# Optimization experiments

Hardware: AMD Instinct MI355X
Metric: run time of the kernel (lower is better)

The kernel has to match this reference:

```python
import jax, jax.numpy as jnp
import numpy as np
import math

BZ, SEQ, NV, VA, HA = 16, 5, 1, 8, 8
C, DSTATE, DCONV, EXPAND, NLAYER = 384, 16, 4, 2, 4
DI = EXPAND * C
DTR = math.ceil(C / 16)  # 24
NTOK = (NV + 2) * SEQ * VA * HA  # 960 multi-modal tokens
T = NTOK + 2                     # + 2 gps tokens


def _ln(x, g, b, eps=1e-5):
    m = jnp.mean(x, -1, keepdims=True)
    v = jnp.mean((x - m) ** 2, -1, keepdims=True)
    return (x - m) * jax.lax.rsqrt(v + eps) * g + b


def _mamba(x, in_w, cw, cb, xw, dtw, dtb, a_log, d, ow):
    # x: (B,T,C); Mamba with bias=False in/out proj, conv_bias=True (mamba_ssm defaults)
    xz = jnp.einsum('btc,ec->bte', x, in_w)            # (B,T,2*DI)
    xh, z = jnp.split(xz, 2, axis=-1)
    xt = jnp.swapaxes(xh, 1, 2)                        # (B,DI,T)
    xt = jax.lax.conv_general_dilated(
        xt, cw[:, None, :], (1,), [(DCONV - 1, 0)],
        feature_group_count=DI, dimension_numbers=('NCH', 'OIH', 'NCH'))
    xh = jax.nn.silu(jnp.swapaxes(xt, 1, 2) + cb)      # causal depthwise conv + SiLU
    xdbl = jnp.einsum('btd,ed->bte', xh, xw)           # (B,T,DTR+2*DS)
    dt, Bm, Cm = jnp.split(xdbl, [DTR, DTR + DSTATE], axis=-1)
    dt = jax.nn.softplus(jnp.einsum('btr,dr->btd', dt, dtw) + dtb)  # (B,T,DI)
    A = -jnp.exp(a_log)                                # (DI,DSTATE)

    def step(h, inp):
        dt_t, x_t, b_t, c_t = inp                      # (B,DI),(B,DI),(B,DS),(B,DS)
        h = h * jnp.exp(dt_t[..., None] * A) + (dt_t * x_t)[..., None] * b_t[:, None, :]
        return h, jnp.einsum('bds,bs->bd', h, c_t)

    h0 = jnp.zeros((x.shape[0], DI, DSTATE), x.dtype)
    xs = tuple(jnp.swapaxes(a, 0, 1) for a in (dt, xh, Bm, Cm))
    _, ys = jax.lax.scan(step, h0, xs)
    y = jnp.swapaxes(ys, 0, 1) + d * xh
    y = y * jax.nn.silu(z)
    return jnp.einsum('btd,cd->btc', y, ow)


def _forward(image_tensor, lidar_tensor, radar_tensor, gps, pos_emb,
             ln1_g, ln1_b, fc1_w, fc1_b, fc2_w, fc2_b,
             in_proj_w, conv_w, conv_b, x_proj_w, dt_proj_w, dt_proj_b,
             A_log, D_param, out_proj_w, ln_f_g, ln_f_b):
    bz = lidar_tensor.shape[0] // SEQ
    h, w = lidar_tensor.shape[2], lidar_tensor.shape[3]
    img = image_tensor.reshape(bz, NV * SEQ, -1, h, w)
    lid = lidar_tensor.reshape(bz, SEQ, -1, h, w)
    rad = radar_tensor.reshape(bz, SEQ, -1, h, w)
    s1, s2 = C // 3, C // 3 * 2
    cs_img = jnp.concatenate([img[:, :, :s1], lid[:, :, s1:s2], rad[:, :, s2:]], axis=2)
    cs_lid = jnp.concatenate([lid[:, :, :s1], rad[:, :, s1:s2], img[:, :, s2:]], axis=2)
    cs_rad = jnp.concatenate([rad[:, :, :s1], img[:, :, s1:s2], lid[:, :, s2:]], axis=2)
    tok = jnp.concatenate([cs_img, cs_lid, cs_rad], axis=1)     # (bz, 3*SEQ, C, h, w)
    tok = jnp.transpose(tok, (0, 1, 3, 4, 2)).reshape(bz, -1, C)
    tok = jnp.concatenate([tok, gps], axis=1)                   # (bz, T, C)
    x = pos_emb + tok                                           # dropout is identity (eval)
    for l in range(NLAYER):
        x_ln = _ln(x, ln1_g[l], ln1_b[l])
        x_fc1 = jnp.einsum('btc,ec->bte', x_ln, fc1_w[l]) + fc1_b[l]
        x_fm = _mamba(x_fc1, in_proj_w[l, 0], conv_w[l, 0], conv_b[l, 0],
                      x_proj_w[l, 0], dt_proj_w[l, 0], dt_proj_b[l, 0],
                      A_log[l, 0], D_param[l, 0], out_proj_w[l, 0])
        x_flip = jnp.flip(x_fc1, axis=1)
        x_bm = _mamba(x_flip, in_proj_w[l, 1], conv_w[l, 1], conv_b[l, 1],
                      x_proj_w[l, 1], dt_proj_w[l, 1], dt_proj_b[l, 1],
                      A_log[l, 1], D_param[l, 1], out_proj_w[l, 1])
        x_fc2 = jnp.einsum('btc,ec->bte', x_flip, fc2_w[l]) + fc2_b[l]
        x_relu = jnp.where(x_fc2 >= 0, x_fc2, 0.2 * x_fc2)      # LeakyReLU(0.2)
        x = x_bm * x_relu + x_fm * x_bm                         # note: x_bm stays flipped, as in original
    x = _ln(x, ln_f_g, ln_f_b)
    pos_out = x[:, NTOK:]
    x = x[:, :NTOK].reshape(bz, (NV + 2) * SEQ, VA, HA, C)
    x = jnp.transpose(x, (0, 1, 4, 2, 3))
    img_out = x[:, :NV * SEQ].reshape(bz * NV * SEQ, -1, h, w)
    lid_out = x[:, NV * SEQ:(NV + 1) * SEQ].reshape(bz * SEQ, -1, h, w)
    rad_out = x[:, (NV + 1) * SEQ:].reshape(bz * SEQ, -1, h, w)
    return img_out, lid_out, rad_out, pos_out


def setup_inputs() -> dict:
    key = jax.random.key(0)
    it = iter(jax.random.split(key, 24))

    def n(shape, s=0.02):
        return jax.random.normal(next(it), shape, jnp.float32) * s

    return dict(
        image_tensor=n((BZ * NV * SEQ, C, VA, HA), 1.0),
        lidar_tensor=n((BZ * SEQ, C, VA, HA), 1.0),
        radar_tensor=n((BZ * SEQ, C, VA, HA), 1.0),
        gps=n((BZ, 2, C), 1.0),
        pos_emb=n((1, T, C), 0.02),
        ln1_g=jnp.ones((NLAYER, C)), ln1_b=jnp.zeros((NLAYER, C)),
        fc1_w=n((NLAYER, C, C)), fc1_b=jnp.zeros((NLAYER, C)),
        fc2_w=n((NLAYER, C, C)), fc2_b=jnp.zeros((NLAYER, C)),
        in_proj_w=n((NLAYER, 2, 2 * DI, C)),
        conv_w=n((NLAYER, 2, DI, DCONV), 0.1),
        conv_b=jnp.zeros((NLAYER, 2, DI)),
        x_proj_w=n((NLAYER, 2, DTR + 2 * DSTATE, DI)),
        dt_proj_w=n((NLAYER, 2, DI, DTR), 0.1),
        dt_proj_b=jnp.full((NLAYER, 2, DI), -4.6, jnp.float32),  # softplus ~ 0.01
        A_log=jnp.tile(jnp.log(jnp.arange(1., DSTATE + 1, dtype=jnp.float32)), (NLAYER, 2, DI, 1)),
        D_param=jnp.ones((NLAYER, 2, DI)),
        out_proj_w=n((NLAYER, 2, C, DI)),
        ln_f_g=jnp.ones((C,)), ln_f_b=jnp.zeros((C,)),
    )


def reference(image_tensor, lidar_tensor, radar_tensor, gps, pos_emb,
              ln1_g, ln1_b, fc1_w, fc1_b, fc2_w, fc2_b,
              in_proj_w, conv_w, conv_b, x_proj_w, dt_proj_w, dt_proj_b,
              A_log, D_param, out_proj_w, ln_f_g, ln_f_b):
    return _forward(image_tensor, lidar_tensor, radar_tensor, gps, pos_emb,
                    ln1_g, ln1_b, fc1_w, fc1_b, fc2_w, fc2_b,
                    in_proj_w, conv_w, conv_b, x_proj_w, dt_proj_w, dt_proj_b,
                    A_log, D_param, out_proj_w, ln_f_g, ln_f_b)
```

## Files before the change

### kernel.cpp

```cpp
#include <hip/hip_runtime.h>
#include <cstdint>
#include <cstddef>


constexpr int BZv = 16, SEQ = 5, NV = 1;
constexpr int C = 384, DSTATE = 16, DCONV = 4, NLAYER = 4;
constexpr int DI = 768;
constexpr int DTR = 24;
constexpr int NTOK = (NV + 2) * SEQ * 64;
constexpr int T = NTOK + 2;
constexpr int M = BZv * T;
constexpr int HB = 8;
constexpr int MH = HB * T;
constexpr int XZdim = 2 * DI;
constexpr int ND = DTR + 2 * DSTATE;
constexpr int NDP = 32;
constexpr int NCHUNK = 26, TC = 37;
constexpr int NQ = 241;
constexpr size_t SEC_SZ = (size_t)BZv * SEQ * C * 64;

typedef __attribute__((ext_vector_type(8))) short short8;
typedef __attribute__((ext_vector_type(4))) float floatx4;

#define GLOAD_LDS16(g, l)                                        \
  __builtin_amdgcn_global_load_lds(                              \
      (const __attribute__((address_space(1))) void*)(g),        \
      (__attribute__((address_space(3))) void*)(l), 16, 0, 0)

__device__ __forceinline__ void split_bf16(float v, short& hi, short& lo) {
  unsigned u = __float_as_uint(v);
  unsigned hib = u & 0xFFFF0000u;
  float r = v - __uint_as_float(hib);
  hi = (short)(hib >> 16);
  lo = (short)(__float_as_uint(r) >> 16);
}

__device__ __forceinline__ float join_bf16(short h, short l) {
  return __uint_as_float((unsigned)(unsigned short)h << 16) +
         __uint_as_float((unsigned)(unsigned short)l << 16);
}

__device__ __forceinline__ void pow16(float e1, float* e) {
  e[0] = e1;
  e[1] = e1 * e1;
  e[3] = e[1] * e[1];
  e[7] = e[3] * e[3];
  e[15] = e[7] * e[7];
  e[2] = e[1] * e[0];
  e[4] = e[3] * e[0];
  e[5] = e[3] * e[1];
  e[6] = e[5] * e[0];
  e[8] = e[7] * e[0];
  e[9] = e[7] * e[1];
  e[10] = e[9] * e[0];
  e[11] = e[7] * e[3];
  e[12] = e[11] * e[0];
  e[13] = e[11] * e[1];
  e[14] = e[13] * e[0];
}

__global__ __launch_bounds__(256) void assemble_k(
    const float* __restrict__ img, const float* __restrict__ lid,
    const float* __restrict__ rad, const float* __restrict__ gps,
    const float* __restrict__ pe, float* __restrict__ x) {
  int idx = blockIdx.x * 256 + threadIdx.x;
  int c = idx % C;
  int m = idx / C;
  int b = m / T, t = m - b * T;
  float v;
  if (t < NTOK) {
    int g_ = t >> 6, p = t & 63;
    int sec = g_ / 5, s = g_ % 5;
    int band = (c < 128) ? 0 : (c < 256 ? 1 : 2);
    int which = (band + sec) % 3;
    const float* src = (which == 0) ? img : (which == 1 ? lid : rad);
    v = src[(((size_t)(b * 5 + s) * C + c) << 6) + p];
  } else {
    v = gps[((size_t)b * 2 + (t - NTOK)) * C + c];
  }
  x[idx] = v + pe[(size_t)t * C + c];
}

__global__ __launch_bounds__(256) void ln_fused_k(
    const float* __restrict__ x, const float* __restrict__ g,
    const float* __restrict__ b, short* __restrict__ oh,
    short* __restrict__ ol) {
  int row = blockIdx.x * 4 + (threadIdx.x >> 6);
  int lane = threadIdx.x & 63;
  const float* xr = x + (size_t)row * C;
  float v[6];
  float s = 0.f;
#pragma unroll
  for (int j = 0; j < 6; j++) {
    v[j] = xr[lane + 64 * j];
    s += v[j];
  }
#pragma unroll
  for (int o = 32; o > 0; o >>= 1) s += __shfl_xor(s, o, 64);
  float mean = s * (1.f / 384.f);
  float q = 0.f;
#pragma unroll
  for (int j = 0; j < 6; j++) {
    float d = v[j] - mean;
    q += d * d;
  }
#pragma unroll
  for (int o = 32; o > 0; o >>= 1) q += __shfl_xor(q, o, 64);
  float rstd = rsqrtf(q * (1.f / 384.f) + 1e-5f);
#pragma unroll
  for (int j = 0; j < 6; j++) {
    int c = lane + 64 * j;
    float val = (v[j] - mean) * rstd * g[c] + b[c];
    short h, l;
    split_bf16(val, h, l);
    oh[(size_t)row * C + c] = h;
    ol[(size_t)row * C + c] = l;
  }
}

__global__ __launch_bounds__(256) void ln_stats2_k(const float* __restrict__ x,
                                                   float* __restrict__ stats) {
  int row = blockIdx.x * 4 + (threadIdx.x >> 6);
  int lane = threadIdx.x & 63;
  const float* xr = x + (size_t)row * C;
  float v[6];
  float s = 0.f;
#pragma unroll
  for (int j = 0; j < 6; j++) {
    v[j] = xr[lane + 64 * j];
    s += v[j];
  }
#pragma unroll
  for (int o = 32; o > 0; o >>= 1) s += __shfl_xor(s, o, 64);
  float mean = s * (1.f / 384.f);
  float q = 0.f;
#pragma unroll
  for (int j = 0; j < 6; j++) {
    float d = v[j] - mean;
    q += d * d;
  }
#pragma unroll
  for (int o = 32; o > 0; o >>= 1) q += __shfl_xor(q, o, 64);
  if (lane == 0) {
    stats[2 * row] = mean;
    stats[2 * row + 1] = rsqrtf(q * (1.f / 384.f) + 1e-5f);
  }
}

__global__ __launch_bounds__(256) void cast_k(const float* __restrict__ src,
                                              int n, short* __restrict__ oh,
                                              short* __restrict__ ol) {
  int idx = blockIdx.x * 256 + threadIdx.x;
  if (idx >= n) return;
  short h, l;
  split_bf16(src[idx], h, l);
  oh[idx] = h;
  ol[idx] = l;
}

__global__ __launch_bounds__(256) void cast_pad_k(const float* __restrict__ src,
                                                  int n, short* __restrict__ oh,
                                                  short* __restrict__ ol) {
  int idx = blockIdx.x * 256 + threadIdx.x;
  if (idx >= n) return;
  int col = idx & 31, row = idx >> 5;
  float v = (col < DTR) ? src[row * DTR + col] : 0.f;
  short h, l;
  split_bf16(v, h, l);
  oh[idx] = h;
  ol[idx] = l;
}

template <int ACT, bool BIAS, bool FLIPA, bool OSPLIT>
__global__ __launch_bounds__(256) void mgemm_k(
    const short* __restrict__ Ah, const short* __restrict__ Al, int K,
    const short* __restrict__ Wh, const short* __restrict__ Wl, int N,
    const float* __restrict__ bias, float* __restrict__ Co, int ldc,
    short* __restrict__ Oh, short* __restrict__ Ol, int Mrows, int arow_off,
    int crow_off) {
  __shared__ __align__(16) short sAh[128 * 32];
  __shared__ __align__(16) short sAl[128 * 32];
  __shared__ __align__(16) short sBh[128 * 32];
  __shared__ __align__(16) short sBl[128 * 32];
  const int tid = threadIdx.x;
  const int wave = tid >> 6, lane = tid & 63;
  const int m0 = blockIdx.y * 128, n0 = blockIdx.x * 128;
  const int lrow = lane >> 2, lchunk = lane & 3;
  const int wm = (wave >> 1) * 64, wn = (wave & 1) * 64;
  const int frow = lane & 15, fquad = lane >> 4;

  size_t arow[2], wrow[2];
#pragma unroll
  for (int p = 0; p < 2; p++) {
    int r = p * 64 + wave * 16 + lrow;
    int lm = m0 + r;
    if (lm >= Mrows) lm = Mrows - 1;
    int g = arow_off + lm;
    if (FLIPA) {
      int bb = g / T;
      int tt = g - bb * T;
      g = bb * T + (T - 1 - tt);
    }
    arow[p] = (size_t)g * K;
    int gn = n0 + r;
    int sn = gn < N ? gn : N - 1;
    wrow[p] = (size_t)sn * K;
  }

  floatx4 acc[4][4] = {};
  for (int k0 = 0; k0 < K; k0 += 32) {
    if (k0) __syncthreads();
    const int kc = k0 + lchunk * 8;
#pragma unroll
    for (int p = 0; p < 2; p++) {
      short* lb = &sAh[(p * 64 + wave * 16) * 32];
      GLOAD_LDS16(Ah + arow[p] + kc, lb);
      lb = &sAl[(p * 64 + wave * 16) * 32];
      GLOAD_LDS16(Al + arow[p] + kc, lb);
      lb = &sBh[(p * 64 + wave * 16) * 32];
      GLOAD_LDS16(Wh + wrow[p] + kc, lb);
      lb = &sBl[(p * 64 + wave * 16) * 32];
      GLOAD_LDS16(Wl + wrow[p] + kc, lb);
    }
    __syncthreads();
    short8 ah[4], al[4], bh[4], bl[4];
#pragma unroll
    for (int i = 0; i < 4; i++) {
      int ra = (wm + i * 16 + frow) * 32 + fquad * 8;
      int rb = (wn + i * 16 + frow) * 32 + fquad * 8;
      ah[i] = *(const short8*)&sAh[ra];
      al[i] = *(const short8*)&sAl[ra];
      bh[i] = *(const short8*)&sBh[rb];
      bl[i] = *(const short8*)&sBl[rb];
    }
#pragma unroll
    for (int i = 0; i < 4; i++)
#pragma unroll
      for (int j = 0; j < 4; j++) {
        acc[i][j] = __builtin_amdgcn_mfma_f32_16x16x32_bf16(ah[i], bh[j],
                                                            acc[i][j], 0, 0, 0);
        acc[i][j] = __builtin_amdgcn_mfma_f32_16x16x32_bf16(al[i], bh[j],
                                                            acc[i][j], 0, 0, 0);
        acc[i][j] = __builtin_amdgcn_mfma_f32_16x16x32_bf16(ah[i], bl[j],
                                                            acc[i][j], 0, 0, 0);
      }
  }
#pragma unroll
  for (int i = 0; i < 4; i++) {
#pragma unroll
    for (int r = 0; r < 4; r++) {
      int gm = m0 + wm + i * 16 + fquad * 4 + r;
      if (gm >= Mrows) continue;
      int grow = crow_off + gm;
#pragma unroll
      for (int j = 0; j < 4; j++) {
        int gn = n0 + wn + j * 16 + frow;
        if (gn >= N) continue;
        float v = acc[i][j][r];
        if constexpr (BIAS) v += bias[gn];
        if constexpr (ACT == 1) v = v >= 0.f ? v : 0.2f * v;
        if constexpr (OSPLIT) {
          short h, l;
          split_bf16(v, h, l);
          Oh[(size_t)grow * N + gn] = h;
          Ol[(size_t)grow * N + gn] = l;
        } else {
          Co[(size_t)grow * ldc + gn] = v;
        }
      }
    }
  }
}

template <int ACT, bool BIAS, int OMODE>
__global__ __launch_bounds__(256) void mgemm64_k(
    const short* __restrict__ Ah, const short* __restrict__ Al, int lda, int K,
    const short* __restrict__ Wh, const short* __restrict__ Wl, int ldw, int N,
    const float* __restrict__ bias, float* __restrict__ Co, int ldc,
    short* __restrict__ Oh, short* __restrict__ Ol, int ldo,
    const float* __restrict__ e1, const float* __restrict__ e2, int Mrows,
    int crow_off) {
  __shared__ __align__(16) short sAh[64 * 32];
  __shared__ __align__(16) short sAl[64 * 32];
  __shared__ __align__(16) short sBh[64 * 32];
  __shared__ __align__(16) short sBl[64 * 32];
  const int tid = threadIdx.x;
  const int wave = tid >> 6, lane = tid & 63;
  const int m0 = blockIdx.y * 64, n0 = blockIdx.x * 64;
  const int srow = tid >> 2, schunk = tid & 3;
  const int frow = lane & 15, fquad = lane >> 4;

  int lm = m0 + srow;
  if (lm >= Mrows) lm = Mrows - 1;
  size_t aoff = (size_t)lm * lda;
  int wn_ = n0 + srow;
  if (wn_ >= N) wn_ = N - 1;
  size_t woff = (size_t)wn_ * ldw;

  floatx4 acc[4] = {};
  for (int k0 = 0; k0 < K; k0 += 32) {
    if (k0) __syncthreads();
    const int kc = k0 + schunk * 8;
    {
      short* lb = &sAh[(wave * 16) * 32];
      GLOAD_LDS16(Ah + aoff + kc, lb);
      lb = &sAl[(wave * 16) * 32];
      GLOAD_LDS16(Al + aoff + kc, lb);
      lb = &sBh[(wave * 16) * 32];
      GLOAD_LDS16(Wh + woff + kc, lb);
      lb = &sBl[(wave * 16) * 32];
      GLOAD_LDS16(Wl + woff + kc, lb);
    }
    __syncthreads();
    short8 ah[4], al[4], bh, bl;
#pragma unroll
    for (int i = 0; i < 4; i++) {
      int ra = (i * 16 + frow) * 32 + fquad * 8;
      ah[i] = *(const short8*)&sAh[ra];
      al[i] = *(const short8*)&sAl[ra];
    }
    {
      int rb = (wave * 16 + frow) * 32 + fquad * 8;
      bh = *(const short8*)&sBh[rb];
      bl = *(const short8*)&sBl[rb];
    }
#pragma unroll
    for (int i = 0; i < 4; i++) {
      acc[i] = __builtin_amdgcn_mfma_f32_16x16x32_bf16(ah[i], bh, acc[i], 0, 0, 0);
      acc[i] = __builtin_amdgcn_mfma_f32_16x16x32_bf16(al[i], bh, acc[i], 0, 0, 0);
      acc[i] = __builtin_amdgcn_mfma_f32_16x16x32_bf16(ah[i], bl, acc[i], 0, 0, 0);
    }
  }
  const int gn = n0 + wave * 16 + frow;
  if (gn < N) {
#pragma unroll
    for (int i = 0; i < 4; i++) {
#pragma unroll
      for (int r = 0; r < 4; r++) {
        int gm = m0 + i * 16 + fquad * 4 + r;
        if (gm >= Mrows) continue;
        int grow = crow_off + gm;
        float v = acc[i][r];
        if constexpr (BIAS) v += bias[gn];
        if constexpr (ACT == 2) v = (v > 20.f) ? v : __logf(1.f + __expf(v));
        if constexpr (ACT == 4) {
          size_t o = (size_t)grow * ldc + gn;
          v = e2[o] * (e1[o] + v);
        }
        if constexpr (OMODE == 1) {
          short h, l;
          split_bf16(v, h, l);
          Oh[(size_t)grow * ldo + gn] = h;
          Ol[(size_t)grow * ldo + gn] = l;
        } else if constexpr (OMODE == 2) {
          if (gn < NDP) {
            short h, l;
            split_bf16(v, h, l);
            Oh[(size_t)grow * NDP + gn] = h;
            Ol[(size_t)grow * NDP + gn] = l;
          }
          if (gn >= DTR) Co[(size_t)grow * 32 + (gn - DTR)] = v;
        } else {
          Co[(size_t)grow * ldc + gn] = v;
        }
      }
    }
  }
}

__global__ __launch_bounds__(256) void conv_k(const float* __restrict__ xz,
                                              const float* __restrict__ cw,
                                              const float* __restrict__ cb,
                                              short* __restrict__ xch,
                                              short* __restrict__ xcl) {
  int idx = blockIdx.x * 256 + threadIdx.x;
  int dh = idx % (DI / 2);
  int rem = idx / (DI / 2);
  int q = rem % NQ;
  int b = rem / NQ;
  int d = dh * 2;
  int t0 = q * 4;
  const float* base = xz + (size_t)b * T * XZdim + d;
  float4 cwa = *(const float4*)&cw[d * 4];
  float4 cwb = *(const float4*)&cw[(d + 1) * 4];
  float cb0 = cb[d], cb1 = cb[d + 1];
  float2 w[7];
#pragma unroll
  for (int j = 0; j < 7; j++) {
    int tt = t0 - 3 + j;
    w[j] = (tt >= 0 && tt < T) ? *(const float2*)(base + (size_t)tt * XZdim)
                               : make_float2(0.f, 0.f);
  }
  const float cwx[4] = {cwa.x, cwa.y, cwa.z, cwa.w};
  const float cwy[4] = {cwb.x, cwb.y, cwb.z, cwb.w};
#pragma unroll
  for (int r = 0; r < 4; r++) {
    int t = t0 + r;
    if (t >= T) break;
    float a0 = cb0, a1 = cb1;
#pragma unroll
    for (int j = 0; j < 4; j++) {
      a0 += w[r + j].x * cwx[j];
      a1 += w[r + j].y * cwy[j];
    }
    float v0 = a0 / (1.f + __expf(-a0));
    float v1 = a1 / (1.f + __expf(-a1));
    short h0, l0, h1, l1;
    split_bf16(v0, h0, l0);
    split_bf16(v1, h1, l1);
    size_t o = ((size_t)b * T + t) * DI + d;
    *(short2*)&xch[o] = make_short2(h0, h1);
    *(short2*)&xcl[o] = make_short2(l0, l1);
  }
}

__global__ __launch_bounds__(256) void scan_p1_k(
    const float* __restrict__ xzb, const short* __restrict__ xch,
    const short* __restrict__ xcl, const float* __restrict__ xdbc,
    const float* __restrict__ alog, float* __restrict__ hchk,
    float* __restrict__ sdt) {
  int d = blockIdx.x * 256 + threadIdx.x;
  int ch = blockIdx.y, b = blockIdx.z;
  float A[DSTATE], h[DSTATE];
  bool powA = true;
#pragma unroll
  for (int s = 0; s < DSTATE; s++) {
    A[s] = -expf(alog[d * DSTATE + s]);
    powA = powA && (fabsf(A[s] + (float)(s + 1)) <= 1e-4f * (float)(s + 1));
    h[s] = 0.f;
  }
  const int t0 = ch * TC;
  const float* xzr = xzb + ((size_t)b * T + t0) * XZdim;
  const short* xchr = xch + ((size_t)b * T + t0) * DI;
  const short* xclr = xcl + ((size_t)b * T + t0) * DI;
  const float* bcr = xdbc + ((size_t)b * T + t0) * 32;
  float sd = 0.f;
  if (powA) {
    for (int t = 0; t < TC; t++) {
      float dt = xzr[(size_t)t * XZdim + d];
      float xv = join_bf16(xchr[(size_t)t * DI + d], xclr[(size_t)t * DI + d]);
      float dx = dt * xv;
      const float* bc = bcr + (size_t)t * 32;
      sd += dt;
      float ev[DSTATE];
      pow16(__expf(-dt), ev);
#pragma unroll
      for (int s = 0; s < DSTATE; s++) h[s] = h[s] * ev[s] + dx * bc[s];
    }
  } else {
    for (int t = 0; t < TC; t++) {
      float dt = xzr[(size_t)t * XZdim + d];
      float xv = join_bf16(xchr[(size_t)t * DI + d], xclr[(size_t)t * DI + d]);
      float dx = dt * xv;
      const float* bc = bcr + (size_t)t * 32;
      sd += dt;
#pragma unroll
      for (int s = 0; s < DSTATE; s++)
        h[s] = h[s] * __expf(dt * A[s]) + dx * bc[s];
    }
  }
  size_t o = ((size_t)(b * NCHUNK + ch) * DSTATE) * DI + d;
#pragma unroll
  for (int s = 0; s < DSTATE; s++) hchk[o + (size_t)s * DI] = h[s];
  sdt[(size_t)(b * NCHUNK + ch) * DI + d] = sd;
}

__global__ __launch_bounds__(256) void scan_p2_k(float* __restrict__ hchk,
                                                 const float* __restrict__ sdt,
                                                 const float* __restrict__ alog) {
  int idx = blockIdx.x * 256 + threadIdx.x;
  int d = idx % DI;
  int rem = idx / DI;
  int s = rem % DSTATE, b = rem / DSTATE;
  float A = -expf(alog[d * DSTATE + s]);
  float hin = 0.f;
#pragma unroll
  for (int ch = 0; ch < NCHUNK; ch++) {
    size_t o = ((size_t)(b * NCHUNK + ch) * DSTATE + s) * DI + d;
    float P = __expf(A * sdt[(size_t)(b * NCHUNK + ch) * DI + d]);
    float hl = hchk[o];
    hchk[o] = hin;
    hin = P * hin + hl;
  }
}

__global__ __launch_bounds__(256) void scan_p3_k(
    const float* __restrict__ xzb, const short* __restrict__ xch,
    const short* __restrict__ xcl, const float* __restrict__ xdbc,
    const float* __restrict__ alog, const float* __restrict__ Dp,
    const float* __restrict__ hchk, short* __restrict__ yh,
    short* __restrict__ yl) {
  int d = blockIdx.x * 256 + threadIdx.x;
  int ch = blockIdx.y, b = blockIdx.z;
  float A[DSTATE], h[DSTATE];
  bool powA = true;
  size_t o = ((size_t)(b * NCHUNK + ch) * DSTATE) * DI + d;
#pragma unroll
  for (int s = 0; s < DSTATE; s++) {
    A[s] = -expf(alog[d * DSTATE + s]);
    powA = powA && (fabsf(A[s] + (float)(s + 1)) <= 1e-4f * (float)(s + 1));
    h[s] = hchk[o + (size_t)s * DI];
  }
  float Dd = Dp[d];
  const int t0 = ch * TC;
  const float* xzr = xzb + ((size_t)b * T + t0) * XZdim;
  const short* xchr = xch + ((size_t)b * T + t0) * DI;
  const short* xclr = xcl + ((size_t)b * T + t0) * DI;
  const float* bcr = xdbc + ((size_t)b * T + t0) * 32;
  if (powA) {
    for (int t = 0; t < TC; t++) {
      float dt = xzr[(size_t)t * XZdim + d];
      float xv = join_bf16(xchr[(size_t)t * DI + d], xclr[(size_t)t * DI + d]);
      float zv = xzr[(size_t)t * XZdim + DI + d];
      float dx = dt * xv;
      float accv = 0.f;
      const float* bc = bcr + (size_t)t * 32;
      float ev[DSTATE];
      pow16(__expf(-dt), ev);
#pragma unroll
      for (int s = 0; s < DSTATE; s++) {
        h[s] = h[s] * ev[s] + dx * bc[s];
        accv += h[s] * bc[DSTATE + s];
      }
      float y = accv + Dd * xv;
      float sz = zv / (1.f + __expf(-zv));
      float v = y * sz;
      short hh, ll;
      split_bf16(v, hh, ll);
      size_t oi = ((size_t)(b * T + t0 + t)) * DI + d;
      yh[oi] = hh;
      yl[oi] = ll;
    }
  } else {
    for (int t = 0; t < TC; t++) {
      float dt = xzr[(size_t)t * XZdim + d];
      float xv = join_bf16(xchr[(size_t)t * DI + d], xclr[(size_t)t * DI + d]);
      float zv = xzr[(size_t)t * XZdim + DI + d];
      float dx = dt * xv;
      float accv = 0.f;
      const float* bc = bcr + (size_t)t * 32;
#pragma unroll
      for (int s = 0; s < DSTATE; s++) {
        h[s] = h[s] * __expf(dt * A[s]) + dx * bc[s];
        accv += h[s] * bc[DSTATE + s];
      }
      float y = accv + Dd * xv;
      float sz = zv / (1.f + __expf(-zv));
      float v = y * sz;
      short hh, ll;
      split_bf16(v, hh, ll);
      size_t oi = ((size_t)(b * T + t0 + t)) * DI + d;
      yh[oi] = hh;
      yl[oi] = ll;
    }
  }
}

__global__ __launch_bounds__(256) void ln_scatter_k(
    const float* __restrict__ x, const float* __restrict__ stats,
    const float* __restrict__ g, const float* __restrict__ bb,
    float* __restrict__ out) {
  __shared__ float lds[64][129];
  int blk = blockIdx.x, tid = threadIdx.x;
  if (blk < 240) {
    int b = blk / 15, g_ = blk % 15;
    int sec = g_ / 5, s = g_ % 5;
    const int rbase = b * T + g_ * 64;
    for (int cc = 0; cc < 3; cc++) {
      if (cc) __syncthreads();
#pragma unroll
      for (int i = 0; i < 32; i++) {
        int lin = tid + 256 * i;
        int p = lin >> 7, c = lin & 127;
        int row = rbase + p;
        int ccc = cc * 128 + c;
        float v = x[(size_t)row * C + ccc];
        v = (v - stats[2 * row]) * stats[2 * row + 1] * g[ccc] + bb[ccc];
        lds[p][c] = v;
      }
      __syncthreads();
      size_t obase = (size_t)sec * SEC_SZ +
                     (((size_t)(b * 5 + s) * C + cc * 128) << 6);
#pragma unroll
      for (int i = 0; i < 32; i++) {
        int lin = tid + 256 * i;
        int c = lin >> 6, p = lin & 63;
        out[obase + ((size_t)c << 6) + p] = lds[p][c];
      }
    }
  } else {
#pragma unroll
    for (int i = 0; i < 48; i++) {
      int lin = tid + 256 * i;
      int r = lin / C, c = lin % C;
      int b = r >> 1, e = r & 1;
      int row = b * T + NTOK + e;
      float v = x[(size_t)row * C + c];
      v = (v - stats[2 * row]) * stats[2 * row + 1] * g[c] + bb[c];
      out[3 * SEC_SZ + ((size_t)(b * 2 + e)) * C + c] = v;
    }
  }
}

extern "C" void kernel_launch(void* const* d_in, const int* in_sizes, int n_in,
                              void* d_out, int out_size, void* d_ws,
                              size_t ws_size, hipStream_t stream) {
  const float* image = (const float*)d_in[0];
  const float* lidar = (const float*)d_in[1];
  const float* radar = (const float*)d_in[2];
  const float* gps = (const float*)d_in[3];
  const float* pe = (const float*)d_in[4];
  const float* ln1g = (const float*)d_in[5];
  const float* ln1b = (const float*)d_in[6];
  const float* fc1w = (const float*)d_in[7];
  const float* fc1b = (const float*)d_in[8];
  const float* fc2w = (const float*)d_in[9];
  const float* fc2b_ = (const float*)d_in[10];
  const float* inw = (const float*)d_in[11];
  const float* cw = (const float*)d_in[12];
  const float* cb = (const float*)d_in[13];
  const float* xw = (const float*)d_in[14];
  const float* dtw = (const float*)d_in[15];
  const float* dtb = (const float*)d_in[16];
  const float* alog = (const float*)d_in[17];
  const float* Dp = (const float*)d_in[18];
  const float* ow = (const float*)d_in[19];
  const float* lnfg = (const float*)d_in[20];
  const float* lnfb = (const float*)d_in[21];
  float* out = (float*)d_out;

  constexpr size_t MC = (size_t)M * C;
  float* ws = (float*)d_ws;
  float* x = ws;
  float* fcb = x + MC;
  float* bmfm = fcb + MC;
  float* x1f = bmfm + MC;
  float* yf = x1f + MC;
  float* xz_h = yf + MC;
  float* xcp = xz_h + (size_t)MH * XZdim;
  float* xdp = xcp + (size_t)MH * DI;
  constexpr size_t CHK_H = (size_t)HB * NCHUNK * DSTATE * DI;
  float* hchk = xdp + (size_t)MH * 64;
  float* sdtb = hchk + CHK_H;
  float* wpl = sdtb + (size_t)HB * NCHUNK * DI;
  float* stats2 = hchk;

  short* lnh = (short*)bmfm;
  short* lnl = lnh + MC;
  float* bm = bmfm;
  short* x1h = (short*)x1f;
  short* x1l = x1h + MC;
  short* yh = (short*)yf;
  short* yl = yh + (size_t)MH * DI;
  short* xch = (short*)xcp;
  short* xcl = xch + (size_t)MH * DI;
  short* xdh = (short*)xdp;
  short* xdl = xdh + (size_t)MH * NDP;
  float* xdbc = xdp + (size_t)MH * 32;

  constexpr size_t WSZ1 = (size_t)NLAYER * C * C;
  constexpr size_t WSZI = (size_t)NLAYER * 2 * 2 * DI * C;
  constexpr size_t WSZO = (size_t)NLAYER * 2 * C * DI;
  constexpr size_t WSZX = (size_t)NLAYER * 2 * ND * DI;
  constexpr size_t WSZD = (size_t)NLAYER * 2 * DI * 32;
  short* wf1h = (short*)wpl;
  short* wf1l = wf1h + WSZ1;
  short* wf2h = wf1l + WSZ1;
  short* wf2l = wf2h + WSZ1;
  short* winh = wf2l + WSZ1;
  short* winl = winh + WSZI;
  short* wowh = winl + WSZI;
  short* wowl = wowh + WSZO;
  short* wxh = wowl + WSZO;
  short* wxl = wxh + WSZX;
  short* wdth = wxl + WSZX;
  short* wdtl = wdth + WSZD;

  cast_k<<<(int)(WSZ1 / 256), 256, 0, stream>>>(fc1w, (int)WSZ1, wf1h, wf1l);
  cast_k<<<(int)(WSZ1 / 256), 256, 0, stream>>>(fc2w, (int)WSZ1, wf2h, wf2l);
  cast_k<<<(int)(WSZI / 256), 256, 0, stream>>>(inw, (int)WSZI, winh, winl);
  cast_k<<<(int)(WSZO / 256), 256, 0, stream>>>(ow, (int)WSZO, wowh, wowl);
  cast_k<<<(int)(WSZX / 256), 256, 0, stream>>>(xw, (int)WSZX, wxh, wxl);
  cast_pad_k<<<(int)(WSZD / 256), 256, 0, stream>>>(dtw, (int)WSZD, wdth, wdtl);

  assemble_k<<<(M * C) / 256, 256, 0, stream>>>(image, lidar, radar, gps, pe, x);

  for (int l = 0; l < NLAYER; l++) {
    ln_fused_k<<<M / 4, 256, 0, stream>>>(x, ln1g + l * C, ln1b + l * C, lnh,
                                          lnl);
    mgemm_k<0, true, false, true><<<dim3(3, 121), 256, 0, stream>>>(
        lnh, lnl, C, wf1h + (size_t)l * C * C, wf1l + (size_t)l * C * C, C,
        fc1b + l * C, nullptr, 0, x1h, x1l, M, 0, 0);
    mgemm_k<1, true, true, false><<<dim3(3, 121), 256, 0, stream>>>(
        x1h, x1l, C, wf2h + (size_t)l * C * C, wf2l + (size_t)l * C * C, C,
        fc2b_ + l * C, fcb, C, nullptr, nullptr, M, 0, 0);
    for (int di = 0; di < 2; di++) {
      const int dir = 1 - di;
      size_t wo = (size_t)(l * 2 + dir);
      for (int h = 0; h < 2; h++) {
        const int roff = h * MH;
        if (dir == 0)
          mgemm_k<0, false, false, false><<<dim3(12, 61), 256, 0, stream>>>(
              x1h, x1l, C, winh + wo * 2 * DI * C, winl + wo * 2 * DI * C,
              2 * DI, nullptr, xz_h, XZdim, nullptr, nullptr, MH, roff, 0);
        else
          mgemm_k<0, false, true, false><<<dim3(12, 61), 256, 0, stream>>>(
              x1h, x1l, C, winh + wo * 2 * DI * C, winl + wo * 2 * DI * C,
              2 * DI, nullptr, xz_h, XZdim, nullptr, nullptr, MH, roff, 0);
        conv_k<<<(HB * NQ * (DI / 2)) / 256, 256, 0, stream>>>(
            xz_h, cw + wo * DI * DCONV, cb + wo * DI, xch, xcl);
        mgemm64_k<0, false, 2><<<dim3(1, 121), 256, 0, stream>>>(
            xch, xcl, DI, DI, wxh + wo * ND * DI, wxl + wo * ND * DI, DI, ND,
            nullptr, xdbc, 0, xdh, xdl, NDP, nullptr, nullptr, MH, 0);
        mgemm64_k<2, true, 0><<<dim3(12, 121), 256, 0, stream>>>(
            xdh, xdl, NDP, 32, wdth + wo * DI * 32, wdtl + wo * DI * 32, 32,
            DI, dtb + wo * DI, xz_h, XZdim, nullptr, nullptr, 0, nullptr,
            nullptr, MH, 0);
        scan_p1_k<<<dim3(3, NCHUNK, HB), 256, 0, stream>>>(
            xz_h, xch, xcl, xdbc, alog + wo * DI * DSTATE, hchk, sdtb);
        scan_p2_k<<<(HB * DSTATE * DI) / 256, 256, 0, stream>>>(
            hchk, sdtb, alog + wo * DI * DSTATE);
        scan_p3_k<<<dim3(3, NCHUNK, HB), 256, 0, stream>>>(
            xz_h, xch, xcl, xdbc, alog + wo * DI * DSTATE, Dp + wo * DI, hchk,
            yh, yl);
        if (dir == 1)
          mgemm64_k<0, false, 0><<<dim3(6, 121), 256, 0, stream>>>(
              yh, yl, DI, DI, wowh + wo * C * DI, wowl + wo * C * DI, DI, C,
              nullptr, bm, C, nullptr, nullptr, 0, nullptr, nullptr, MH, roff);
        else
          mgemm64_k<4, false, 0><<<dim3(6, 121), 256, 0, stream>>>(
              yh, yl, DI, DI, wowh + wo * C * DI, wowl + wo * C * DI, DI, C,
              nullptr, x, C, nullptr, nullptr, 0, fcb, bm, MH, roff);
      }
    }
  }
  ln_stats2_k<<<M / 4, 256, 0, stream>>>(x, stats2);
  ln_scatter_k<<<241, 256, 0, stream>>>(x, stats2, lnfg, lnfb, out);
}
```

Baseline: 3.123 ms.

## Double-buffer GEMM shared-memory tiles and transpose input assembly through LDS

Both split-bf16 MFMA GEMM kernels now use two LDS buffers. The next K-slice's global-to-LDS loads are issued right after the barrier, so they overlap with the MFMA work on the current slice instead of stalling before it. The assemble kernel now reads each 64-token by 128-channel source block coalesced, transposes it through padded shared memory, and writes rows of x coalesced; one extra block handles the GPS tokens. The cost is double the LDS per GEMM block, up to 64KB for the 128-tile kernel, which can reduce occupancy.

```diff
diff --git a/kernel.cpp b/kernel.cpp
--- a/kernel.cpp
+++ b/kernel.cpp
@@ -63,22 +63,42 @@
     const float* __restrict__ img, const float* __restrict__ lid,
     const float* __restrict__ rad, const float* __restrict__ gps,
     const float* __restrict__ pe, float* __restrict__ x) {
-  int idx = blockIdx.x * 256 + threadIdx.x;
-  int c = idx % C;
-  int m = idx / C;
-  int b = m / T, t = m - b * T;
-  float v;
-  if (t < NTOK) {
-    int g_ = t >> 6, p = t & 63;
+  __shared__ float lds[64][129];
+  int blk = blockIdx.x, tid = threadIdx.x;
+  if (blk < 240) {
+    int b = blk / 15, g_ = blk % 15;
     int sec = g_ / 5, s = g_ % 5;
-    int band = (c < 128) ? 0 : (c < 256 ? 1 : 2);
-    int which = (band + sec) % 3;
-    const float* src = (which == 0) ? img : (which == 1 ? lid : rad);
-    v = src[(((size_t)(b * 5 + s) * C + c) << 6) + p];
+    for (int cc = 0; cc < 3; cc++) {
+      if (cc) __syncthreads();
+      int which = (cc + sec) % 3;
+      const float* src = (which == 0) ? img : (which == 1 ? lid : rad);
+      size_t sbase = (((size_t)(b * 5 + s) * C + cc * 128) << 6);
+#pragma unroll
+      for (int i = 0; i < 32; i++) {
+        int lin = tid + 256 * i;
+        int p = lin & 63, cl = lin >> 6;
+        lds[p][cl] = src[sbase + lin];
+      }
+      __syncthreads();
+#pragma unroll
+      for (int i = 0; i < 32; i++) {
+        int lin = tid + 256 * i;
+        int cl = lin & 127, p = lin >> 7;
+        int t = g_ * 64 + p;
+        int c = cc * 128 + cl;
+        x[((size_t)b * T + t) * C + c] = lds[p][cl] + pe[(size_t)t * C + c];
+      }
+    }
   } else {
-    v = gps[((size_t)b * 2 + (t - NTOK)) * C + c];
-  }
-  x[idx] = v + pe[(size_t)t * C + c];
+#pragma unroll
+    for (int i = 0; i < 48; i++) {
+      int lin = tid + 256 * i;
+      int r = lin / C, c = lin % C;
+      int b = r >> 1, e = r & 1;
+      x[((size_t)b * T + NTOK + e) * C + c] =
+          gps[((size_t)b * 2 + e) * C + c] + pe[(size_t)(NTOK + e) * C + c];
+    }
+  }
 }
 
 __global__ __launch_bounds__(256) void ln_fused_k(
@@ -178,10 +198,10 @@
     const float* __restrict__ bias, float* __restrict__ Co, int ldc,
     short* __restrict__ Oh, short* __restrict__ Ol, int Mrows, int arow_off,
     int crow_off) {
-  __shared__ __align__(16) short sAh[128 * 32];
-  __shared__ __align__(16) short sAl[128 * 32];
-  __shared__ __align__(16) short sBh[128 * 32];
-  __shared__ __align__(16) short sBl[128 * 32];
+  __shared__ __align__(16) short sAh[2][128 * 32];
+  __shared__ __align__(16) short sAl[2][128 * 32];
+  __shared__ __align__(16) short sBh[2][128 * 32];
+  __shared__ __align__(16) short sBl[2][128 * 32];
   const int tid = threadIdx.x;
   const int wave = tid >> 6, lane = tid & 63;
   const int m0 = blockIdx.y * 128, n0 = blockIdx.x * 128;
@@ -207,31 +227,34 @@
     wrow[p] = (size_t)sn * K;
   }
 
+  const int lo = (wave * 16) * 32;
+  auto issue = [&](int k0, int buf) {
+    const int kc = k0 + lchunk * 8;
+#pragma unroll
+    for (int p = 0; p < 2; p++) {
+      GLOAD_LDS16(Ah + arow[p] + kc, &sAh[buf][p * 64 * 32 + lo]);
+      GLOAD_LDS16(Al + arow[p] + kc, &sAl[buf][p * 64 * 32 + lo]);
+      GLOAD_LDS16(Wh + wrow[p] + kc, &sBh[buf][p * 64 * 32 + lo]);
+      GLOAD_LDS16(Wl + wrow[p] + kc, &sBl[buf][p * 64 * 32 + lo]);
+    }
+  };
+
+  issue(0, 0);
+  const int nsteps = K / 32;
   floatx4 acc[4][4] = {};
-  for (int k0 = 0; k0 < K; k0 += 32) {
-    if (k0) __syncthreads();
-    const int kc = k0 + lchunk * 8;
-#pragma unroll
-    for (int p = 0; p < 2; p++) {
-      short* lb = &sAh[(p * 64 + wave * 16) * 32];
-      GLOAD_LDS16(Ah + arow[p] + kc, lb);
-      lb = &sAl[(p * 64 + wave * 16) * 32];
-      GLOAD_LDS16(Al + arow[p] + kc, lb);
-      lb = &sBh[(p * 64 + wave * 16) * 32];
-      GLOAD_LDS16(Wh + wrow[p] + kc, lb);
-      lb = &sBl[(p * 64 + wave * 16) * 32];
-      GLOAD_LDS16(Wl + wrow[p] + kc, lb);
-    }
+  for (int ks = 0; ks < nsteps; ks++) {
+    const int buf = ks & 1;
     __syncthreads();
+    if (ks + 1 < nsteps) issue((ks + 1) * 32, 1 - buf);
     short8 ah[4], al[4], bh[4], bl[4];
 #pragma unroll
     for (int i = 0; i < 4; i++) {
       int ra = (wm + i * 16 + frow) * 32 + fquad * 8;
       int rb = (wn + i * 16 + frow) * 32 + fquad * 8;
-      ah[i] = *(const short8*)&sAh[ra];
-      al[i] = *(const short8*)&sAl[ra];
-      bh[i] = *(const short8*)&sBh[rb];
-      bl[i] = *(const short8*)&sBl[rb];
+      ah[i] = *(const short8*)&sAh[buf][ra];
+      al[i] = *(const short8*)&sAl[buf][ra];
+      bh[i] = *(const short8*)&sBh[buf][rb];
+      bl[i] = *(const short8*)&sBl[buf][rb];
     }
 #pragma unroll
     for (int i = 0; i < 4; i++)
@@ -280,10 +303,10 @@
     short* __restrict__ Oh, short* __restrict__ Ol, int ldo,
     const float* __restrict__ e1, const float* __restrict__ e2, int Mrows,
     int crow_off) {
-  __shared__ __align__(16) short sAh[64 * 32];
-  __shared__ __align__(16) short sAl[64 * 32];
-  __shared__ __align__(16) short sBh[64 * 32];
-  __shared__ __align__(16) short sBl[64 * 32];
+  __shared__ __align__(16) short sAh[2][64 * 32];
+  __shared__ __align__(16) short sAl[2][64 * 32];
+  __shared__ __align__(16) short sBh[2][64 * 32];
+  __shared__ __align__(16) short sBl[2][64 * 32];
   const int tid = threadIdx.x;
   const int wave = tid >> 6, lane = tid & 63;
   const int m0 = blockIdx.y * 64, n0 = blockIdx.x * 64;
@@ -297,32 +320,33 @@
   if (wn_ >= N) wn_ = N - 1;
   size_t woff = (size_t)wn_ * ldw;
 
+  const int lo = (wave * 16) * 32;
+  auto issue = [&](int k0, int buf) {
+    const int kc = k0 + schunk * 8;
+    GLOAD_LDS16(Ah + aoff + kc, &sAh[buf][lo]);
+    GLOAD_LDS16(Al + aoff + kc, &sAl[buf][lo]);
+    GLOAD_LDS16(Wh + woff + kc, &sBh[buf][lo]);
+    GLOAD_LDS16(Wl + woff + kc, &sBl[buf][lo]);
+  };
+
+  issue(0, 0);
+  const int nsteps = K / 32;
   floatx4 acc[4] = {};
-  for (int k0 = 0; k0 < K; k0 += 32) {
-    if (k0) __syncthreads();
-    const int kc = k0 + schunk * 8;
-    {
-      short* lb = &sAh[(wave * 16) * 32];
-      GLOAD_LDS16(Ah + aoff + kc, lb);
-      lb = &sAl[(wave * 16) * 32];
-      GLOAD_LDS16(Al + aoff + kc, lb);
-      lb = &sBh[(wave * 16) * 32];
-      GLOAD_LDS16(Wh + woff + kc, lb);
-      lb = &sBl[(wave * 16) * 32];
-      GLOAD_LDS16(Wl + woff + kc, lb);
-    }
+  for (int ks = 0; ks < nsteps; ks++) {
+    const int buf = ks & 1;
     __syncthreads();
+    if (ks + 1 < nsteps) issue((ks + 1) * 32, 1 - buf);
     short8 ah[4], al[4], bh, bl;
 #pragma unroll
     for (int i = 0; i < 4; i++) {
       int ra = (i * 16 + frow) * 32 + fquad * 8;
-      ah[i] = *(const short8*)&sAh[ra];
-      al[i] = *(const short8*)&sAl[ra];
+      ah[i] = *(const short8*)&sAh[buf][ra];
+      al[i] = *(const short8*)&sAl[buf][ra];
     }
     {
       int rb = (wave * 16 + frow) * 32 + fquad * 8;
-      bh = *(const short8*)&sBh[rb];
-      bl = *(const short8*)&sBl[rb];
+      bh = *(const short8*)&sBh[buf][rb];
+      bl = *(const short8*)&sBl[buf][rb];
     }
 #pragma unroll
     for (int i = 0; i < 4; i++) {
@@ -683,7 +707,7 @@
   cast_k<<<(int)(WSZX / 256), 256, 0, stream>>>(xw, (int)WSZX, wxh, wxl);
   cast_pad_k<<<(int)(WSZD / 256), 256, 0, stream>>>(dtw, (int)WSZD, wdth, wdtl);
 
-  assemble_k<<<(M * C) / 256, 256, 0, stream>>>(image, lidar, radar, gps, pe, x);
+  assemble_k<<<241, 256, 0, stream>>>(image, lidar, radar, gps, pe, x);
 
   for (int l = 0; l < NLAYER; l++) {
     ln_fused_k<<<M / 4, 256, 0, stream>>>(x, ln1g + l * C, ln1b + l * C, lnh,
```

New measurement: 3.185 ms. 1.02x slower.
